# Performance work log

Measured on AMD Instinct MI355X. Metric: run time of the kernel, lower is better.

Reference implementation:

```python
import jax, jax.numpy as jnp
import numpy as np

K = 7          # involution kernel size
GC = 16        # group_channels (hardcoded in module)
BN_EPS = 1e-5
LN_EPS = 1e-6


def _forward(x, conv1_w, conv1_b, bn_gamma, bn_beta, bn_mean, bn_var,
             conv2_w, conv2_b, ln_w, ln_b, w1, b1, w2, b2):
    b, c, h, w = x.shape
    groups = c // GC
    # --- involution: dynamic kernel generation (1x1 conv -> BN(eval) -> ReLU -> 1x1 conv) ---
    t = jnp.einsum('bchw,oc->bohw', x, conv1_w) + conv1_b[None, :, None, None]
    t = (t - bn_mean[None, :, None, None]) * (bn_gamma / jnp.sqrt(bn_var + BN_EPS))[None, :, None, None] \
        + bn_beta[None, :, None, None]
    t = jax.nn.relu(t)
    wgt = jnp.einsum('bchw,oc->bohw', t, conv2_w) + conv2_b[None, :, None, None]
    wgt = wgt.reshape(b, groups, K * K, h, w)                  # (b,g,k2,h,w)
    # --- unfold: gather kxk neighborhoods (channel-major, then kh, kw — matches torch Unfold) ---
    p = (K - 1) // 2
    xp = jnp.pad(x, ((0, 0), (0, 0), (p, p), (p, p)))
    patches = jnp.stack([xp[:, :, i:i + h, j:j + w]
                         for i in range(K) for j in range(K)], axis=2)   # (b,c,k2,h,w)
    patches = patches.reshape(b, groups, GC, K * K, h, w)
    # weighted sum over kernel positions
    out = jnp.einsum('bgkhw,bgckhw->bgchw', wgt, patches).reshape(b, c, h, w)
    # --- LN + MLP residual (channels_last) ---
    y = out.transpose(0, 2, 3, 1)                               # (b,h,w,c)
    mu = y.mean(-1, keepdims=True)
    var = ((y - mu) ** 2).mean(-1, keepdims=True)
    y = (y - mu) / jnp.sqrt(var + LN_EPS) * ln_w + ln_b
    y = jax.nn.gelu(y @ w1.T + b1, approximate=False)           # torch GELU = exact erf
    y = y @ w2.T + b2                                           # dropout_rate=0 -> identity
    return y.transpose(0, 3, 1, 2) + x


def setup_inputs() -> dict:
    key = jax.random.key(0)
    ks = jax.random.split(key, 6)
    dim = 128
    groups = dim // GC
    red = dim // 4
    b, h, w = 8, 56, 56
    return {
        'x': jax.random.normal(ks[0], (b, dim, h, w), jnp.float32),
        'conv1_w': jax.random.normal(ks[1], (red, dim), jnp.float32) * (1.0 / np.sqrt(dim)),
        'conv1_b': jnp.zeros((red,), jnp.float32),
        'bn_gamma': jnp.ones((red,), jnp.float32),
        'bn_beta': jnp.zeros((red,), jnp.float32),
        'bn_mean': jnp.zeros((red,), jnp.float32),
        'bn_var': jnp.ones((red,), jnp.float32),
        'conv2_w': jax.random.normal(ks[2], (K * K * groups, red), jnp.float32) * (1.0 / np.sqrt(red)),
        'conv2_b': jnp.zeros((K * K * groups,), jnp.float32),
        'ln_w': jnp.ones((dim,), jnp.float32),
        'ln_b': jnp.zeros((dim,), jnp.float32),
        'w1': jax.random.normal(ks[3], (4 * dim, dim), jnp.float32) * (1.0 / np.sqrt(dim)),
        'b1': jnp.zeros((4 * dim,), jnp.float32),
        'w2': jax.random.normal(ks[4], (dim, 4 * dim), jnp.float32) * (1.0 / np.sqrt(4 * dim)),
        'b2': jnp.zeros((dim,), jnp.float32),
    }


def reference(x, conv1_w, conv1_b, bn_gamma, bn_beta, bn_mean, bn_var,
              conv2_w, conv2_b, ln_w, ln_b, w1, b1, w2, b2):
    return _forward(x, conv1_w, conv1_b, bn_gamma, bn_beta, bn_mean, bn_var,
                    conv2_w, conv2_b, ln_w, ln_b, w1, b1, w2, b2)
```

## Files before the change

### kernel.cpp

```cpp
#include <hip/hip_runtime.h>
#include <hip/hip_bf16.h>
#include <math.h>

#define HW    3136
#define WIMG  56
#define NPIX  25088
#define CIN   128
#define RED   32
#define NGROUP 8
#define GCH   16
#define KKK   49

typedef __attribute__((ext_vector_type(8))) short short8;
typedef __attribute__((ext_vector_type(4))) float f32x4;
typedef unsigned short ushort_t;

static __device__ __forceinline__ unsigned int f2b(float f) {
    union { __hip_bfloat16 b; unsigned short u; } cv;
    cv.b = __float2bfloat16(f);
    return (unsigned int)cv.u;
}

static __device__ __forceinline__ float gelu_t(float h) {
    float z = h * fmaf(0.0356774081f, h * h, 0.7978845608f);
    float e = __expf(-2.f * z);
    return __fdividef(h, 1.f + e);
}

__global__ __launch_bounds__(256) void k_prep(const float* __restrict__ conv1_w,
    const float* __restrict__ conv1_b, const float* __restrict__ bn_g,
    const float* __restrict__ bn_b, const float* __restrict__ bn_m,
    const float* __restrict__ bn_v, const float* __restrict__ conv2_w,
    const float* __restrict__ ln_w, const float* __restrict__ w1,
    const float* __restrict__ w2,
    ushort_t* __restrict__ c1b, ushort_t* __restrict__ c2b,
    ushort_t* __restrict__ lw1b, ushort_t* __restrict__ w2b,
    float* __restrict__ sc1, float* __restrict__ sh1)
{
    int id = blockIdx.x * 256 + threadIdx.x;
    w2b[id] = (ushort_t)f2b(w2[id]);
    int c = id & 127;
    lw1b[id] = (ushort_t)f2b(w1[id] * ln_w[c]);
    if (id < 4096)  c1b[id] = (ushort_t)f2b(conv1_w[id]);
    if (id < 12800) c2b[id] = (id < 12544) ? (ushort_t)f2b(conv2_w[id]) : (ushort_t)0;
    if (id < 32) {
        float sc = bn_g[id] * rsqrtf(bn_v[id] + 1e-5f);
        sc1[id] = sc;
        sh1[id] = (conv1_b[id] - bn_m[id]) * sc + bn_b[id];
    }
}

__global__ void k_prep2(const float* __restrict__ w1, const float* __restrict__ ln_w,
    const float* __restrict__ ln_b, const float* __restrict__ b1,
    float* __restrict__ s1, float* __restrict__ t1)
{
    int n = threadIdx.x;
    const float* wr = w1 + (size_t)n * 128;
    float s = 0.f, t = 0.f;
    #pragma unroll 8
    for (int c = 0; c < 128; ++c) { float w = wr[c]; s += ln_w[c] * w; t += ln_b[c] * w; }
    s1[n] = s; t1[n] = t + b1[n];
}

__global__ __launch_bounds__(256) void k_mega(const float* __restrict__ x,
    const short* __restrict__ c1b, const short* __restrict__ c2b,
    const float* __restrict__ sc1, const float* __restrict__ sh1,
    const float* __restrict__ c2bias,
    const ushort_t* __restrict__ lw1b, const ushort_t* __restrict__ w2b,
    const float* __restrict__ s1, const float* __restrict__ t1,
    const float* __restrict__ b2, float* __restrict__ outp)
{
    __shared__ __align__(16) char smem[80960];
    short* swg  = (short*)smem;
    short* sh   = (short*)smem;
    short* sx   = (short*)smem + 26656;
    short* st   = (short*)(smem + 70720);
    float* sred  = (float*)(smem + 70720);
    float* sred2 = sred + 1280;

    int tid  = threadIdx.x;
    int bid  = blockIdx.x;
    int sblk = (bid & 7) * 49 + (bid >> 3);
    int P0   = sblk * 64;
    int b    = P0 / HW;
    int p0i  = P0 - b * HW;
    int lane = tid & 63, wv = tid >> 6;
    int ln15 = lane & 15, quad = lane >> 4;

    const float* xb = x + (size_t)b * CIN * HW + p0i;
    #pragma unroll
    for (int it = 0; it < 32; ++it) {
        int idx = it * 256 + tid;
        int c = idx >> 6, pp = idx & 63;
        sx[pp * 136 + c] = (short)f2b(xb[(size_t)c * HW + pp]);
    }
    __syncthreads();

    f32x4 acc1c[2] = {(f32x4)0.f, (f32x4)0.f};
    #pragma unroll
    for (int kc = 0; kc < 128; kc += 32) {
        short8 af = *(const short8*)&sx[(wv * 16 + ln15) * 136 + kc + quad * 8];
        #pragma unroll
        for (int nt = 0; nt < 2; ++nt) {
            short8 bf = *(const short8*)&c1b[(size_t)(nt * 16 + ln15) * 128 + kc + quad * 8];
            acc1c[nt] = __builtin_amdgcn_mfma_f32_16x16x32_bf16(af, bf, acc1c[nt], 0, 0, 0);
        }
    }
    #pragma unroll
    for (int nt = 0; nt < 2; ++nt) {
        int o = nt * 16 + ln15;
        float sc = sc1[o], shv = sh1[o];
        #pragma unroll
        for (int r = 0; r < 4; ++r) {
            float tv = fmaxf(acc1c[nt][r] * sc + shv, 0.f);
            st[(wv * 16 + quad * 4 + r) * 40 + o] = (short)f2b(tv);
        }
    }
    short8 af2 = *(const short8*)&st[(wv * 16 + ln15) * 40 + quad * 8];
    f32x4 zc = (f32x4)0.f;
    #pragma unroll
    for (int nt = 0; nt < 25; ++nt) {
        int gk = nt * 16 + ln15;
        short8 bf2 = *(const short8*)&c2b[(size_t)gk * 32 + quad * 8];
        f32x4 a2 = __builtin_amdgcn_mfma_f32_16x16x32_bf16(af2, bf2, zc, 0, 0, 0);
        if (gk < 392) {
            float bj = c2bias[gk];
            uint2 pk;
            pk.x = f2b(a2[0] + bj) | (f2b(a2[1] + bj) << 16);
            pk.y = f2b(a2[2] + bj) | (f2b(a2[3] + bj) << 16);
            *(uint2*)&swg[gk * 68 + wv * 16 + quad * 4] = pk;
        }
    }
    __syncthreads();

    {
        int q   = tid & 15;
        int gy  = tid >> 4;
        int g   = gy >> 1;
        int sub = gy & 1;
        int pl0 = q * 4;
        int p   = p0i + pl0;
        int prow = p / WIMG;
        int pcol = p - prow * WIMG;
        const float* xc = x + ((size_t)b * CIN + g * GCH + sub * 8) * HW;
        float acc[4][8];
        #pragma unroll
        for (int i = 0; i < 4; ++i)
            #pragma unroll
            for (int c = 0; c < 8; ++c) acc[i][c] = 0.f;
        bool c_lo = (pcol >= 4);
        bool c_hi = (pcol <= 48);
        #pragma unroll
        for (int dy = -3; dy <= 3; ++dy) {
            int grow = prow + dy;
            if (grow < 0 || grow >= WIMG) continue;
            float wkf[7][4];
            #pragma unroll
            for (int dx = 0; dx < 7; ++dx) {
                int gk = g * KKK + (dy + 3) * 7 + dx;
                uint2 wld = *(const uint2*)&swg[gk * 68 + pl0];
                wkf[dx][0] = __uint_as_float(wld.x << 16);
                wkf[dx][1] = __uint_as_float(wld.x & 0xffff0000u);
                wkf[dx][2] = __uint_as_float(wld.y << 16);
                wkf[dx][3] = __uint_as_float(wld.y & 0xffff0000u);
            }
            const float* xrow = xc + grow * WIMG + pcol;
            #pragma unroll
            for (int c = 0; c < 8; ++c) {
                const float* xr = xrow + (size_t)c * HW;
                float4 v0 = c_lo ? *(const float4*)(xr - 4) : make_float4(0.f,0.f,0.f,0.f);
                float4 v1 = *(const float4*)(xr);
                float4 v2 = c_hi ? *(const float4*)(xr + 4) : make_float4(0.f,0.f,0.f,0.f);
                float vv[12] = {v0.x,v0.y,v0.z,v0.w, v1.x,v1.y,v1.z,v1.w, v2.x,v2.y,v2.z,v2.w};
                #pragma unroll
                for (int dx = 0; dx < 7; ++dx)
                    #pragma unroll
                    for (int i = 0; i < 4; ++i)
                        acc[i][c] += wkf[dx][i] * vv[i + dx + 1];
            }
        }
        #pragma unroll
        for (int i = 0; i < 4; ++i) {
            unsigned pk[4];
            float s = 0.f, s2 = 0.f;
            #pragma unroll
            for (int h = 0; h < 4; ++h)
                pk[h] = f2b(acc[i][2*h]) | (f2b(acc[i][2*h+1]) << 16);
            #pragma unroll
            for (int c = 0; c < 8; ++c) { s += acc[i][c]; s2 += acc[i][c] * acc[i][c]; }
            *(uint4*)&sx[(pl0 + i) * 136 + g * 16 + sub * 8] = make_uint4(pk[0],pk[1],pk[2],pk[3]);
            sred [(pl0 + i) * 20 + gy] = s;
            sred2[(pl0 + i) * 20 + gy] = s2;
        }
    }
    __syncthreads();

    float mu_r[4], rs_r[4];
    #pragma unroll
    for (int tn = 0; tn < 4; ++tn) {
        int px = tn * 16 + ln15;
        float s = 0.f, s2 = 0.f;
        #pragma unroll
        for (int k4 = 0; k4 < 4; ++k4) {
            float4 a = *(const float4*)&sred [px * 20 + k4 * 4];
            float4 c = *(const float4*)&sred2[px * 20 + k4 * 4];
            s  += a.x + a.y + a.z + a.w;
            s2 += c.x + c.y + c.z + c.w;
        }
        float m = s * (1.f / 128.f);
        mu_r[tn] = m;
        rs_r[tn] = rsqrtf(s2 * (1.f / 128.f) - m * m + 1e-6f);
    }

    f32x4 acc2[4][2];
    #pragma unroll
    for (int i = 0; i < 4; ++i)
        #pragma unroll
        for (int j = 0; j < 2; ++j) acc2[i][j] = (f32x4)0.f;

    for (int j = 0; j < 4; ++j) {
        short8 a1f[4][2], b2f[4][2];
        #pragma unroll
        for (int k4 = 0; k4 < 4; ++k4) {
            #pragma unroll
            for (int tm = 0; tm < 2; ++tm)
                a1f[k4][tm] = *(const short8*)&lw1b[(size_t)(j * 128 + wv * 32 + tm * 16 + ln15) * 128 + k4 * 32 + quad * 8];
            #pragma unroll
            for (int tn = 0; tn < 2; ++tn)
                b2f[k4][tn] = *(const short8*)&w2b[(size_t)(wv * 32 + tn * 16 + ln15) * 512 + j * 128 + k4 * 32 + quad * 8];
        }
        f32x4 acc1[2][4];
        #pragma unroll
        for (int tm = 0; tm < 2; ++tm)
            #pragma unroll
            for (int tn = 0; tn < 4; ++tn) acc1[tm][tn] = (f32x4)0.f;
        #pragma unroll
        for (int k4 = 0; k4 < 4; ++k4) {
            short8 bf[4];
            #pragma unroll
            for (int tn = 0; tn < 4; ++tn)
                bf[tn] = *(const short8*)&sx[(tn * 16 + ln15) * 136 + k4 * 32 + quad * 8];
            #pragma unroll
            for (int tm = 0; tm < 2; ++tm)
                #pragma unroll
                for (int tn = 0; tn < 4; ++tn)
                    acc1[tm][tn] = __builtin_amdgcn_mfma_f32_16x16x32_bf16(a1f[k4][tm], bf[tn], acc1[tm][tn], 0, 0, 0);
        }
        #pragma unroll
        for (int tm = 0; tm < 2; ++tm) {
            int nl = wv * 32 + tm * 16 + quad * 4;
            int n  = j * 128 + nl;
            float4 s14 = *(const float4*)&s1[n];
            float4 t14 = *(const float4*)&t1[n];
            #pragma unroll
            for (int tn = 0; tn < 4; ++tn) {
                int px = tn * 16 + ln15;
                float g0 = gelu_t(rs_r[tn] * (acc1[tm][tn][0] - mu_r[tn] * s14.x) + t14.x);
                float g1 = gelu_t(rs_r[tn] * (acc1[tm][tn][1] - mu_r[tn] * s14.y) + t14.y);
                float g2 = gelu_t(rs_r[tn] * (acc1[tm][tn][2] - mu_r[tn] * s14.z) + t14.z);
                float g3 = gelu_t(rs_r[tn] * (acc1[tm][tn][3] - mu_r[tn] * s14.w) + t14.w);
                uint2 pk;
                pk.x = f2b(g0) | (f2b(g1) << 16);
                pk.y = f2b(g2) | (f2b(g3) << 16);
                *(uint2*)&sh[px * 136 + nl] = pk;
            }
        }
        __syncthreads();
        #pragma unroll
        for (int k4 = 0; k4 < 4; ++k4) {
            short8 af[4];
            #pragma unroll
            for (int tm = 0; tm < 4; ++tm)
                af[tm] = *(const short8*)&sh[(tm * 16 + ln15) * 136 + k4 * 32 + quad * 8];
            #pragma unroll
            for (int tm = 0; tm < 4; ++tm)
                #pragma unroll
                for (int tn = 0; tn < 2; ++tn)
                    acc2[tm][tn] = __builtin_amdgcn_mfma_f32_16x16x32_bf16(af[tm], b2f[k4][tn], acc2[tm][tn], 0, 0, 0);
        }
        __syncthreads();
    }

    #pragma unroll
    for (int tm = 0; tm < 4; ++tm) {
        int p = p0i + tm * 16 + quad * 4;
        #pragma unroll
        for (int tn = 0; tn < 2; ++tn) {
            int c = wv * 32 + tn * 16 + ln15;
            size_t base = ((size_t)b * CIN + c) * HW + p;
            float bj = b2[c];
            float4 rv = *(const float4*)&x[base];
            float4 ov = make_float4(acc2[tm][tn][0] + bj + rv.x,
                                    acc2[tm][tn][1] + bj + rv.y,
                                    acc2[tm][tn][2] + bj + rv.z,
                                    acc2[tm][tn][3] + bj + rv.w);
            *(float4*)&outp[base] = ov;
        }
    }
}

extern "C" void kernel_launch(void* const* d_in, const int* in_sizes, int n_in,
                              void* d_out, int out_size, void* d_ws, size_t ws_size,
                              hipStream_t stream) {
    const float* x       = (const float*)d_in[0];
    const float* conv1_w = (const float*)d_in[1];
    const float* conv1_b = (const float*)d_in[2];
    const float* bn_g    = (const float*)d_in[3];
    const float* bn_b    = (const float*)d_in[4];
    const float* bn_m    = (const float*)d_in[5];
    const float* bn_v    = (const float*)d_in[6];
    const float* conv2_w = (const float*)d_in[7];
    const float* conv2_b = (const float*)d_in[8];
    const float* ln_w    = (const float*)d_in[9];
    const float* ln_b    = (const float*)d_in[10];
    const float* w1      = (const float*)d_in[11];
    const float* b1      = (const float*)d_in[12];
    const float* w2      = (const float*)d_in[13];
    const float* b2      = (const float*)d_in[14];
    float* out = (float*)d_out;

    float* F = (float*)d_ws;
    float* sc1  = F;
    float* sh1  = F + 32;
    float* s1   = F + 64;
    float* t1   = F + 576;
    ushort_t* S    = (ushort_t*)(F + 1088);
    ushort_t* c1b  = S;
    ushort_t* c2b  = c1b + 4096;
    ushort_t* lw1b = c2b + 12800;
    ushort_t* w2b  = lw1b + 65536;

    k_prep <<<256, 256, 0, stream>>>(conv1_w, conv1_b, bn_g, bn_b, bn_m, bn_v,
                                     conv2_w, ln_w, w1, w2, c1b, c2b, lw1b, w2b, sc1, sh1);
    k_prep2<<<1, 512, 0, stream>>>(w1, ln_w, ln_b, b1, s1, t1);
    k_mega <<<392, 256, 0, stream>>>(x, (const short*)c1b, (const short*)c2b,
                                     sc1, sh1, conv2_b, lw1b, w2b, s1, t1, b2, out);
}
```

Before: 153.3 us.

## Double-buffer MLP hidden tile to skew GEMM2 behind GEMM1 and drop a barrier

The MLP loop now keeps two LDS buffers for the GELU hidden tile. In each iteration, GEMM2 on the previous chunk runs interleaved with GEMM1 for the current chunk, with a tail step for the last chunk, which removes one __syncthreads per iteration. The c2b weight fragments are also prefetched into registers before the kernel-generation MFMA loop, and launch_bounds now requests 2 blocks per CU. In exchange, register pressure rises from the unrolled loops and the 25-element fragment array, which could cause spills, and the extra LDS buffer overlaps regions that must stay free.

Result: faster. 147.4 us (-3.9%).

```diff
diff --git a/kernel.cpp b/kernel.cpp
--- a/kernel.cpp
+++ b/kernel.cpp
@@ -62,7 +62,7 @@
     s1[n] = s; t1[n] = t + b1[n];
 }
 
-__global__ __launch_bounds__(256) void k_mega(const float* __restrict__ x,
+__global__ __launch_bounds__(256, 2) void k_mega(const float* __restrict__ x,
     const short* __restrict__ c1b, const short* __restrict__ c2b,
     const float* __restrict__ sc1, const float* __restrict__ sh1,
     const float* __restrict__ c2bias,
@@ -72,7 +72,8 @@
 {
     __shared__ __align__(16) char smem[80960];
     short* swg  = (short*)smem;
-    short* sh   = (short*)smem;
+    short* sh0  = (short*)smem;
+    short* sh1b = (short*)smem + 8704;
     short* sx   = (short*)smem + 26656;
     short* st   = (short*)(smem + 70720);
     float* sred  = (float*)(smem + 70720);
@@ -116,19 +117,24 @@
             st[(wv * 16 + quad * 4 + r) * 40 + o] = (short)f2b(tv);
         }
     }
-    short8 af2 = *(const short8*)&st[(wv * 16 + ln15) * 40 + quad * 8];
-    f32x4 zc = (f32x4)0.f;
-    #pragma unroll
-    for (int nt = 0; nt < 25; ++nt) {
-        int gk = nt * 16 + ln15;
-        short8 bf2 = *(const short8*)&c2b[(size_t)gk * 32 + quad * 8];
-        f32x4 a2 = __builtin_amdgcn_mfma_f32_16x16x32_bf16(af2, bf2, zc, 0, 0, 0);
-        if (gk < 392) {
-            float bj = c2bias[gk];
-            uint2 pk;
-            pk.x = f2b(a2[0] + bj) | (f2b(a2[1] + bj) << 16);
-            pk.y = f2b(a2[2] + bj) | (f2b(a2[3] + bj) << 16);
-            *(uint2*)&swg[gk * 68 + wv * 16 + quad * 4] = pk;
+    {
+        short8 af2 = *(const short8*)&st[(wv * 16 + ln15) * 40 + quad * 8];
+        short8 bf2[25];
+        #pragma unroll
+        for (int nt = 0; nt < 25; ++nt)
+            bf2[nt] = *(const short8*)&c2b[(size_t)(nt * 16 + ln15) * 32 + quad * 8];
+        f32x4 zc = (f32x4)0.f;
+        #pragma unroll
+        for (int nt = 0; nt < 25; ++nt) {
+            int gk = nt * 16 + ln15;
+            f32x4 a2 = __builtin_amdgcn_mfma_f32_16x16x32_bf16(af2, bf2[nt], zc, 0, 0, 0);
+            if (gk < 392) {
+                float bj = c2bias[gk];
+                uint2 pk;
+                pk.x = f2b(a2[0] + bj) | (f2b(a2[1] + bj) << 16);
+                pk.y = f2b(a2[2] + bj) | (f2b(a2[3] + bj) << 16);
+                *(uint2*)&swg[gk * 68 + wv * 16 + quad * 4] = pk;
+            }
         }
     }
     __syncthreads();
@@ -218,16 +224,35 @@
         #pragma unroll
         for (int j = 0; j < 2; ++j) acc2[i][j] = (f32x4)0.f;
 
+    #pragma unroll
     for (int j = 0; j < 4; ++j) {
-        short8 a1f[4][2], b2f[4][2];
-        #pragma unroll
-        for (int k4 = 0; k4 < 4; ++k4) {
+        short* shc = (j & 1) ? sh1b : sh0;
+        short* shp = (j & 1) ? sh0  : sh1b;
+        short8 a1f[4][2];
+        #pragma unroll
+        for (int k4 = 0; k4 < 4; ++k4)
             #pragma unroll
             for (int tm = 0; tm < 2; ++tm)
                 a1f[k4][tm] = *(const short8*)&lw1b[(size_t)(j * 128 + wv * 32 + tm * 16 + ln15) * 128 + k4 * 32 + quad * 8];
-            #pragma unroll
-            for (int tn = 0; tn < 2; ++tn)
-                b2f[k4][tn] = *(const short8*)&w2b[(size_t)(wv * 32 + tn * 16 + ln15) * 512 + j * 128 + k4 * 32 + quad * 8];
+        if (j > 0) {
+            short8 bq[4][2];
+            #pragma unroll
+            for (int k4 = 0; k4 < 4; ++k4)
+                #pragma unroll
+                for (int tn = 0; tn < 2; ++tn)
+                    bq[k4][tn] = *(const short8*)&w2b[(size_t)(wv * 32 + tn * 16 + ln15) * 512 + (j - 1) * 128 + k4 * 32 + quad * 8];
+            #pragma unroll
+            for (int k4 = 0; k4 < 4; ++k4) {
+                short8 af[4];
+                #pragma unroll
+                for (int tm = 0; tm < 4; ++tm)
+                    af[tm] = *(const short8*)&shp[(tm * 16 + ln15) * 136 + k4 * 32 + quad * 8];
+                #pragma unroll
+                for (int tm = 0; tm < 4; ++tm)
+                    #pragma unroll
+                    for (int tn = 0; tn < 2; ++tn)
+                        acc2[tm][tn] = __builtin_amdgcn_mfma_f32_16x16x32_bf16(af[tm], bq[k4][tn], acc2[tm][tn], 0, 0, 0);
+            }
         }
         f32x4 acc1[2][4];
         #pragma unroll
@@ -262,23 +287,30 @@
                 uint2 pk;
                 pk.x = f2b(g0) | (f2b(g1) << 16);
                 pk.y = f2b(g2) | (f2b(g3) << 16);
-                *(uint2*)&sh[px * 136 + nl] = pk;
+                *(uint2*)&shc[px * 136 + nl] = pk;
             }
         }
         __syncthreads();
+    }
+    {
+        short8 bq[4][2];
+        #pragma unroll
+        for (int k4 = 0; k4 < 4; ++k4)
+            #pragma unroll
+            for (int tn = 0; tn < 2; ++tn)
+                bq[k4][tn] = *(const short8*)&w2b[(size_t)(wv * 32 + tn * 16 + ln15) * 512 + 3 * 128 + k4 * 32 + quad * 8];
         #pragma unroll
         for (int k4 = 0; k4 < 4; ++k4) {
             short8 af[4];
             #pragma unroll
             for (int tm = 0; tm < 4; ++tm)
-                af[tm] = *(const short8*)&sh[(tm * 16 + ln15) * 136 + k4 * 32 + quad * 8];
+                af[tm] = *(const short8*)&sh1b[(tm * 16 + ln15) * 136 + k4 * 32 + quad * 8];
             #pragma unroll
             for (int tm = 0; tm < 4; ++tm)
                 #pragma unroll
                 for (int tn = 0; tn < 2; ++tn)
-                    acc2[tm][tn] = __builtin_amdgcn_mfma_f32_16x16x32_bf16(af[tm], b2f[k4][tn], acc2[tm][tn], 0, 0, 0);
-        }
-        __syncthreads();
+                    acc2[tm][tn] = __builtin_amdgcn_mfma_f32_16x16x32_bf16(af[tm], bq[k4][tn], acc2[tm][tn], 0, 0, 0);
+        }
     }
 
     #pragma unroll
```
